# Kernel tuning notes

Hardware: AMD Instinct MI355X
Metric: run time of the kernel (lower is better)

The kernel has to match this reference:

```python
import jax, jax.numpy as jnp
import numpy as np

DEPTH = 4
HIDDEN = 256
ATOM_FDIM = 143
BOND_FDIM = 14
N_ATOMS = 65536
N_BONDS = 131072
MAX_NB = 6
ATOMS_PER_MOL = 32


def setup_inputs() -> dict:
    key = jax.random.key(0)
    ks = jax.random.split(key, 12)
    s = 0.05  # weight init scale
    return {
        'fatoms': jax.random.uniform(ks[0], (N_ATOMS, ATOM_FDIM), dtype=jnp.float32),
        'fbonds': jax.random.uniform(ks[1], (N_BONDS, ATOM_FDIM + BOND_FDIM), dtype=jnp.float32),
        'agraph': jax.random.randint(ks[2], (N_ATOMS, MAX_NB), 0, N_BONDS, dtype=jnp.int32),
        'bgraph': jax.random.randint(ks[3], (N_BONDS, MAX_NB), 0, N_BONDS, dtype=jnp.int32),
        'atoms_per_mol': ATOMS_PER_MOL,
        'W_i': jax.random.normal(ks[4], (ATOM_FDIM + BOND_FDIM, HIDDEN), dtype=jnp.float32) * s,
        'W_h': jax.random.normal(ks[5], (HIDDEN, HIDDEN), dtype=jnp.float32) * s,
        'W_o_w': jax.random.normal(ks[6], (ATOM_FDIM + HIDDEN, HIDDEN), dtype=jnp.float32) * s,
        'W_o_b': jax.random.normal(ks[7], (HIDDEN,), dtype=jnp.float32) * s,
        'W_a': jax.random.normal(ks[8], (HIDDEN, HIDDEN), dtype=jnp.float32) * s,
        'W_b_w': jax.random.normal(ks[9], (HIDDEN, HIDDEN), dtype=jnp.float32) * s,
        'W_b_b': jax.random.normal(ks[10], (HIDDEN,), dtype=jnp.float32) * s,
        'W_ma1': jax.random.normal(ks[11], (HIDDEN, 1), dtype=jnp.float32) * s,
    }


def reference(fatoms, fbonds, agraph, bgraph, atoms_per_mol,
              W_i, W_h, W_o_w, W_o_b, W_a, W_b_w, W_b_b, W_ma1):
    act = jax.nn.relu  # activation == 'ReLU'; dropout == 0 (identity)

    binput = fbonds @ W_i                      # [E, H]
    message = act(binput)
    for _ in range(DEPTH - 1):
        nei = message[bgraph]                  # [E, max_nb, H] gather
        # message attention over incoming messages (softmax over neighbor axis)
        att = jax.nn.softmax(nei @ W_ma1, axis=1)  # [E, max_nb, 1]
        nei = (nei * att).sum(axis=1)          # [E, H]
        message = act(binput + nei @ W_h)

    nei_a = message[agraph].sum(axis=1)        # [N, H]
    ainput = jnp.concatenate([fatoms, nei_a], axis=1)
    atom_h = act(ainput @ W_o_w + W_o_b)       # [N, H]

    # per-molecule self-attention pooling; equal-size molecules -> batched
    A = atoms_per_mol
    B = atom_h.shape[0] // A
    h = atom_h.reshape(B, A, HIDDEN)           # [B, A, H]
    scores = jnp.einsum('bad,bcd->bac', h @ W_a, h)   # [B, A, A]
    att_w = jax.nn.softmax(scores, axis=-1)
    att_h = act(jnp.einsum('bac,bcd->bad', att_w, h) @ W_b_w + W_b_b)
    mol_vecs = (h + att_h).sum(axis=1) / A     # [B, H]
    return mol_vecs
```

## Files before the change

kernel.cpp:

```cpp
#include <hip/hip_runtime.h>

typedef unsigned short u16;
typedef __attribute__((ext_vector_type(8))) short short8;
typedef __attribute__((ext_vector_type(4))) float floatx4;
typedef __attribute__((ext_vector_type(4), aligned(4))) float floatx4u;

__device__ __forceinline__ float bf2f(u16 u) {
    return __uint_as_float(((unsigned int)u) << 16);
}
__device__ __forceinline__ u16 f2bf(float f) {
    unsigned int i = __float_as_uint(f);
    unsigned int r = i + 0x7FFFu + ((i >> 16) & 1u);
    return (u16)(r >> 16);
}
__device__ __forceinline__ unsigned int relu2(unsigned int x) {
    unsigned int m = (((x >> 15) & 1u) * 0x0000FFFFu) | ((x >> 31) * 0xFFFF0000u);
    return x & ~m;
}

typedef __attribute__((address_space(3))) void lds_void;
typedef const __attribute__((address_space(1))) void g_void;
__device__ __forceinline__ void async_copy16(const void* g, void* l) {
    __builtin_amdgcn_global_load_lds((g_void*)g, (lds_void*)l, 16, 0, 0);
}

__device__ __forceinline__ void acc_bf8(float* a8, uint4 u, float wj) {
    a8[0] += wj * __uint_as_float(u.x << 16);
    a8[1] += wj * __uint_as_float(u.x & 0xffff0000u);
    a8[2] += wj * __uint_as_float(u.y << 16);
    a8[3] += wj * __uint_as_float(u.y & 0xffff0000u);
    a8[4] += wj * __uint_as_float(u.z << 16);
    a8[5] += wj * __uint_as_float(u.z & 0xffff0000u);
    a8[6] += wj * __uint_as_float(u.w << 16);
    a8[7] += wj * __uint_as_float(u.w & 0xffff0000u);
}

#define MFMA16(a, b, c) __builtin_amdgcn_mfma_f32_16x16x32_bf16(a, b, c, 0, 0, 0)

#define E_BONDS 131072
#define N_ATOMS_C 65536
#define KPAD_I 160
#define KPAD_O 416
#define N_MOLS 2048

__global__ __launch_bounds__(256) void prep_wt(const float* __restrict__ W, u16* __restrict__ Wt, int K, int Kpad) {
    int idx = blockIdx.x * 256 + threadIdx.x;
    int n = idx / Kpad;
    int k = idx - n * Kpad;
    float v = (k < K) ? W[(size_t)k * 256 + n] : 0.f;
    Wt[idx] = f2bf(v);
}

__global__ __launch_bounds__(256) void prep_wo(const float* __restrict__ W, u16* __restrict__ Wt) {
    int idx = blockIdx.x * 256 + threadIdx.x;
    int n = idx / KPAD_O;
    int k = idx - n * KPAD_O;
    float v = 0.f;
    if (k < 256)      v = W[(size_t)(143 + k) * 256 + n];
    else if (k < 399) v = W[(size_t)(k - 256) * 256 + n];
    Wt[idx] = f2bf(v);
}

template <int EPI, bool RELUA, bool F32A>
__global__ __launch_bounds__(512, 3) void gemm256(
    const u16* __restrict__ A, const u16* __restrict__ Bt,
    u16* __restrict__ out,
    const float* __restrict__ bias, const float* __restrict__ wma,
    float* __restrict__ tout, int K, const float* __restrict__ Af32)
{
    __shared__ char ldsbuf[33792];
    u16* Al = (u16*)ldsbuf;
    u16* Bl = (u16*)(ldsbuf + 8192);

    const int tid = threadIdx.x;
    const int w = tid >> 6, lane = tid & 63;
    const int quad = lane >> 4, mr = lane & 15;
    const int m0 = blockIdx.x * 128;

    floatx4 acc[16] = {};

    const u16* Ag = F32A ? nullptr : (A + (size_t)(m0 + (tid & 127)) * K + ((tid >> 7) << 3));
    const float* Af = F32A ? (Af32 + (size_t)(m0 + (tid >> 2)) * 157) : nullptr;

    for (int k0 = 0; k0 < K; k0 += 32) {
        if (F32A) {
            const int kb = tid & 3;
            const int cb = k0 + kb * 8;
            short8 xv;
            if (cb + 8 <= 157) {
                floatx4u v0 = *(const floatx4u*)(Af + cb);
                floatx4u v1 = *(const floatx4u*)(Af + cb + 4);
                xv[0] = (short)f2bf(v0.x); xv[1] = (short)f2bf(v0.y);
                xv[2] = (short)f2bf(v0.z); xv[3] = (short)f2bf(v0.w);
                xv[4] = (short)f2bf(v1.x); xv[5] = (short)f2bf(v1.y);
                xv[6] = (short)f2bf(v1.z); xv[7] = (short)f2bf(v1.w);
            } else {
#pragma unroll
                for (int e = 0; e < 8; ++e) {
                    int c = cb + e;
                    float v = (c < 157) ? Af[c] : 0.f;
                    xv[e] = (short)f2bf(v);
                }
            }
            *(short8*)(Al + ((kb << 7) + (tid >> 2)) * 8) = xv;
        } else if (RELUA) {
            uint4 x = *(const uint4*)(Ag + k0);
            x.x = relu2(x.x); x.y = relu2(x.y); x.z = relu2(x.z); x.w = relu2(x.w);
            *(uint4*)(Al + tid * 8) = x;
        } else {
            async_copy16(Ag + k0, Al + tid * 8);
        }
#pragma unroll
        for (int i = 0; i < 2; ++i) {
            int c = tid + i * 512;
            async_copy16(Bt + (size_t)(c & 255) * K + k0 + ((c >> 8) << 3), Bl + c * 8);
        }
        __syncthreads();

        short8 af = *(const short8*)(Al + quad * 1024 + (w * 16 + mr) * 8);
#pragma unroll
        for (int j = 0; j < 16; ++j) {
            short8 bf = *(const short8*)(Bl + quad * 2048 + (j * 16 + mr) * 8);
            acc[j] = MFMA16(af, bf, acc[j]);
        }
        __syncthreads();
    }

    u16* slice = (u16*)ldsbuf + w * 2112;
    const int lhalf = lane >> 5;
    const int lcol = (lane & 31) * 8;
    float wmal8[8];
    if (EPI == 1) {
#pragma unroll
        for (int e = 0; e < 8; ++e) wmal8[e] = wma[lcol + e];
    }
    float bl16[16];
    if (EPI == 3) {
#pragma unroll
        for (int j = 0; j < 16; ++j) bl16[j] = bias[j * 16 + mr];
    }

#pragma unroll
    for (int p = 0; p < 2; ++p) {
        if ((quad >> 1) == p) {
            int lr = (quad & 1) * 4;
#pragma unroll
            for (int j = 0; j < 16; ++j)
#pragma unroll
                for (int r = 0; r < 4; ++r) {
                    float v = acc[j][r];
                    if (EPI == 3) { v += bl16[j]; v = v > 0.f ? v : 0.f; }
                    slice[(lr + r) * 264 + j * 16 + mr] = f2bf(v);
                }
        }
        __syncthreads();
#pragma unroll
        for (int round = 0; round < 4; ++round) {
            int rowl = round * 2 + lhalf;
            int row = m0 + w * 16 + p * 8 + rowl;
            size_t off = (size_t)row * 256 + lcol;
            short8 pv = *(const short8*)(slice + rowl * 264 + lcol);
            if (EPI == 0 || EPI == 3) {
                *(short8*)(out + off) = pv;
            } else {
                *(short8*)(out + off) = pv;
                float pdot = 0.f;
#pragma unroll
                for (int e = 0; e < 8; ++e) {
                    u16 u = (u16)pv[e];
                    u = (u & 0x8000u) ? (u16)0 : u;
                    pdot += bf2f(u) * wmal8[e];
                }
                pdot += __shfl_xor(pdot, 1); pdot += __shfl_xor(pdot, 2);
                pdot += __shfl_xor(pdot, 4); pdot += __shfl_xor(pdot, 8);
                pdot += __shfl_xor(pdot, 16);
                if ((lane & 31) == 0) tout[row] = pdot;
            }
        }
        __syncthreads();
    }
}

template <int MODE>
__global__ __launch_bounds__(512, 6) void fused_gg(
    const u16* src, const u16* __restrict__ Bt, const int* __restrict__ graph,
    const float* __restrict__ t_in, const u16* __restrict__ binput,
    const float* __restrict__ fatoms, const float* __restrict__ bias,
    const float* __restrict__ wma, u16* __restrict__ outp, float* __restrict__ t_out)
{
    constexpr int MT = (MODE == 2) ? 32 : 64;
    constexpr int KK = (MODE == 2) ? 416 : 256;
    constexpr int KP = KK + 8;
    constexpr int MF = MT / 16;
    constexpr int LDSB = (MODE == 2) ? (32 * 424 * 2) : (32 * 268 * 4);

    __shared__ __align__(16) char ldsbuf[LDSB];
    u16* As = (u16*)ldsbuf;

    const int tid = threadIdx.x;
    const int w = tid >> 6, lane = tid & 63;
    const int quad = lane >> 4, mr = lane & 15;
    const int hw = tid >> 5, l32 = tid & 31;
    const int m0 = blockIdx.x * MT;

    for (int it = 0; it < MT / 16; ++it) {
        const int r = it * 16 + hw;
        const int e = m0 + r;
        const int* bg = graph + (size_t)e * 6;
        int2 b01 = *(const int2*)bg;
        int2 b23 = *(const int2*)(bg + 2);
        int2 b45 = *(const int2*)(bg + 4);
        int b[6] = {b01.x, b01.y, b23.x, b23.y, b45.x, b45.y};

        float wg[6];
        if (MODE != 2) {
            float s[6];
#pragma unroll
            for (int j = 0; j < 6; ++j) s[j] = t_in[b[j]];
            float mx = fmaxf(fmaxf(fmaxf(s[0], s[1]), fmaxf(s[2], s[3])), fmaxf(s[4], s[5]));
            float den = 0.f;
#pragma unroll
            for (int j = 0; j < 6; ++j) { wg[j] = __expf(s[j] - mx); den += wg[j]; }
            float inv = 1.f / den;
#pragma unroll
            for (int j = 0; j < 6; ++j) wg[j] *= inv;
        }

        float a8[8] = {};
#pragma unroll
        for (int j = 0; j < 6; ++j) {
            uint4 u = *(const uint4*)(src + (size_t)b[j] * 256 + l32 * 8);
            if (MODE == 1) { u.x = relu2(u.x); u.y = relu2(u.y); u.z = relu2(u.z); u.w = relu2(u.w); }
            acc_bf8(a8, u, (MODE == 2) ? 1.f : wg[j]);
        }
        short8 mv;
#pragma unroll
        for (int k = 0; k < 8; ++k) mv[k] = (short)f2bf(a8[k]);
        *(short8*)(As + r * KP + l32 * 8) = mv;

        if (MODE == 2) {
            const float* frow = fatoms + (size_t)e * 143;
#pragma unroll
            for (int i = 0; i < 5; ++i) {
                int c = l32 + i * 32;
                As[r * KP + 256 + c] = (c < 143) ? f2bf(frow[c]) : (u16)0;
            }
        }
    }
    __syncthreads();

    floatx4 acc[MF][2] = {};
    const u16* bp0 = Bt + (size_t)(w * 32 + mr) * KK + quad * 8;
    const u16* bp1 = bp0 + (size_t)16 * KK;
#pragma unroll 2
    for (int ks = 0; ks < KK / 32; ++ks) {
        const int k0 = ks * 32;
        short8 bf0 = *(const short8*)(bp0 + k0);
        short8 bf1 = *(const short8*)(bp1 + k0);
#pragma unroll
        for (int mf = 0; mf < MF; ++mf) {
            short8 af = *(const short8*)(As + (mf * 16 + mr) * KP + k0 + quad * 8);
            acc[mf][0] = MFMA16(af, bf0, acc[mf][0]);
            acc[mf][1] = MFMA16(af, bf1, acc[mf][1]);
        }
    }
    __syncthreads();

    if (MODE != 2) {
        float* Pf = (float*)ldsbuf;
        const int rrow = tid >> 4;
        const int rcol = (tid & 15) * 16;
        float wv[16];
#pragma unroll
        for (int e2 = 0; e2 < 16; ++e2) wv[e2] = wma[rcol + e2];

#pragma unroll
        for (int p = 0; p < 2; ++p) {
#pragma unroll
            for (int mi = 0; mi < 2; ++mi) {
#pragma unroll
                for (int jj = 0; jj < 2; ++jj)
#pragma unroll
                    for (int r = 0; r < 4; ++r)
                        Pf[(mi * 16 + quad * 4 + r) * 268 + (w * 2 + jj) * 16 + mr] = acc[p * 2 + mi][jj][r];
            }
            __syncthreads();
            const int grow = m0 + p * 32 + rrow;
            const u16* brow = binput + (size_t)grow * 256 + rcol;
            uint4 bu0 = *(const uint4*)brow;
            uint4 bu1 = *(const uint4*)(brow + 8);
            float bv[16] = {
                __uint_as_float(bu0.x << 16), __uint_as_float(bu0.x & 0xffff0000u),
                __uint_as_float(bu0.y << 16), __uint_as_float(bu0.y & 0xffff0000u),
                __uint_as_float(bu0.z << 16), __uint_as_float(bu0.z & 0xffff0000u),
                __uint_as_float(bu0.w << 16), __uint_as_float(bu0.w & 0xffff0000u),
                __uint_as_float(bu1.x << 16), __uint_as_float(bu1.x & 0xffff0000u),
                __uint_as_float(bu1.y << 16), __uint_as_float(bu1.y & 0xffff0000u),
                __uint_as_float(bu1.z << 16), __uint_as_float(bu1.z & 0xffff0000u),
                __uint_as_float(bu1.w << 16), __uint_as_float(bu1.w & 0xffff0000u)};
            const float* prow = Pf + rrow * 268 + rcol;
            float pdot = 0.f;
            short8 o0, o1;
#pragma unroll
            for (int e2 = 0; e2 < 16; ++e2) {
                float v = prow[e2] + bv[e2];
                v = v > 0.f ? v : 0.f;
                u16 q = f2bf(v);
                if (e2 < 8) o0[e2] = (short)q; else o1[e2 - 8] = (short)q;
                pdot += bf2f(q) * wv[e2];
            }
            size_t off = (size_t)grow * 256 + rcol;
            *(short8*)(outp + off) = o0;
            *(short8*)(outp + off + 8) = o1;
            pdot += __shfl_xor(pdot, 1); pdot += __shfl_xor(pdot, 2);
            pdot += __shfl_xor(pdot, 4); pdot += __shfl_xor(pdot, 8);
            if ((lane & 15) == 0) t_out[grow] = pdot;
            __syncthreads();
        }
    } else {
        u16* Pu = (u16*)ldsbuf;
        float bl0 = bias[(w * 2 + 0) * 16 + mr];
        float bl1 = bias[(w * 2 + 1) * 16 + mr];
#pragma unroll
        for (int mf = 0; mf < MF; ++mf)
#pragma unroll
            for (int r = 0; r < 4; ++r) {
                float v0 = acc[mf][0][r] + bl0; v0 = v0 > 0.f ? v0 : 0.f;
                float v1 = acc[mf][1][r] + bl1; v1 = v1 > 0.f ? v1 : 0.f;
                Pu[(mf * 16 + quad * 4 + r) * 264 + (w * 2 + 0) * 16 + mr] = f2bf(v0);
                Pu[(mf * 16 + quad * 4 + r) * 264 + (w * 2 + 1) * 16 + mr] = f2bf(v1);
            }
        __syncthreads();
        const int rrow = tid >> 4;
        const int rcol = (tid & 15) * 16;
        size_t off = (size_t)(m0 + rrow) * 256 + rcol;
        short8 v0 = *(const short8*)(Pu + rrow * 264 + rcol);
        short8 v1 = *(const short8*)(Pu + rrow * 264 + rcol + 8);
        *(short8*)(outp + off) = v0;
        *(short8*)(outp + off + 8) = v1;
    }
}

#define HSTR 260
__global__ __launch_bounds__(256) void mol_attn(const u16* __restrict__ atomh, const u16* __restrict__ hWg,
                                                u16* __restrict__ z) {
    __shared__ float hs[32 * HSTR];
    __shared__ float P[32 * 33];
    const int t = threadIdx.x;
    const int b = blockIdx.x;
    const u16* hbase = atomh + (size_t)b * 32 * 256;
    for (int e0 = t * 4; e0 < 8192; e0 += 1024) {
        int row = e0 >> 8, col = e0 & 255;
        ushort4 u = *(const ushort4*)(hbase + e0);
        floatx4 v; v.x = bf2f(u.x); v.y = bf2f(u.y); v.z = bf2f(u.z); v.w = bf2f(u.w);
        *(floatx4*)&hs[row * HSTR + col] = v;
    }
    __syncthreads();

    {
        int c = t & 31, a0 = t >> 5;
        const u16* hWb = hWg + (size_t)b * 32 * 256;
        for (int r = 0; r < 4; ++r) {
            int a = a0 + r * 8;
            const u16* hwrow = hWb + a * 256;
            float s = 0.f;
            for (int d = 0; d < 256; d += 4) {
                ushort4 u = *(const ushort4*)(hwrow + d);
                const float* hp = &hs[c * HSTR + d];
                s += bf2f(u.x) * hp[0] + bf2f(u.y) * hp[1] + bf2f(u.z) * hp[2] + bf2f(u.w) * hp[3];
            }
            P[a * 33 + c] = s;
        }
    }
    __syncthreads();
    if (t < 32) {
        float* prow = &P[t * 33];
        float mx = prow[0];
        for (int i = 1; i < 32; ++i) mx = fmaxf(mx, prow[i]);
        float den = 0.f;
        for (int i = 0; i < 32; ++i) { float ev = __expf(prow[i] - mx); prow[i] = ev; den += ev; }
        float inv = 1.f / den;
        for (int i = 0; i < 32; ++i) prow[i] *= inv;
    }
    __syncthreads();

    {
        int a = t >> 3, q = t & 7;
        floatx4 acc8[8];
#pragma unroll
        for (int i = 0; i < 8; ++i) acc8[i] = (floatx4){0.f, 0.f, 0.f, 0.f};
        const float* prow = &P[a * 33];
        for (int cc = 0; cc < 32; ++cc) {
            float p = prow[cc];
            const float* hrow = &hs[cc * HSTR + q * 4];
#pragma unroll
            for (int i = 0; i < 8; ++i) {
                floatx4 hv = *(const floatx4*)(hrow + i * 32);
                acc8[i] += p * hv;
            }
        }
        u16* zrow = z + ((size_t)b * 32 + a) * 256 + q * 4;
#pragma unroll
        for (int i = 0; i < 8; ++i) {
            ushort4 o;
            o.x = f2bf(acc8[i].x); o.y = f2bf(acc8[i].y); o.z = f2bf(acc8[i].z); o.w = f2bf(acc8[i].w);
            *(ushort4*)(zrow + i * 32) = o;
        }
    }
}

__global__ __launch_bounds__(256) void final_reduce(const u16* __restrict__ atomh, const u16* __restrict__ atth,
                                                    float* __restrict__ out) {
    int idx = blockIdx.x * 256 + threadIdx.x;
    int b = idx >> 8, d = idx & 255;
    const u16* ph = atomh + ((size_t)b * 32) * 256 + d;
    const u16* pa = atth + ((size_t)b * 32) * 256 + d;
    float s = 0.f;
#pragma unroll 4
    for (int a = 0; a < 32; ++a) s += bf2f(ph[a * 256]) + bf2f(pa[a * 256]);
    out[idx] = s * 0.03125f;
}

#define O_FBP      ((size_t)0)
#define O_BINPUT   ((size_t)41943040)
#define O_MSGA     ((size_t)109051904)
#define O_MSGB     ((size_t)176160768)
#define O_W        ((size_t)243269632)
#define O_WTI      (O_W)
#define O_WTH      (O_W + 81920)
#define O_WTO      (O_W + 212992)
#define O_WTA      (O_W + 425984)
#define O_WTB      (O_W + 557056)
#define WS_NEED    ((size_t)243957760)

extern "C" void kernel_launch(void* const* d_in, const int* in_sizes, int n_in,
                              void* d_out, int out_size, void* d_ws, size_t ws_size,
                              hipStream_t stream) {
    const float* fatoms = (const float*)d_in[0];
    const float* fbonds = (const float*)d_in[1];
    const int*   agraph = (const int*)d_in[2];
    const int*   bgraph = (const int*)d_in[3];
    const float* W_i    = (const float*)d_in[5];
    const float* W_h    = (const float*)d_in[6];
    const float* W_o_w  = (const float*)d_in[7];
    const float* W_o_b  = (const float*)d_in[8];
    const float* W_a    = (const float*)d_in[9];
    const float* W_b_w  = (const float*)d_in[10];
    const float* W_b_b  = (const float*)d_in[11];
    const float* W_ma1  = (const float*)d_in[12];
    float* out = (float*)d_out;

    if (ws_size < WS_NEED) return;

    char* ws = (char*)d_ws;
    u16* binput  = (u16*)(ws + O_BINPUT);
    u16* msgA    = (u16*)(ws + O_MSGA);
    u16* msgB    = (u16*)(ws + O_MSGB);
    u16* wti     = (u16*)(ws + O_WTI);
    u16* wth     = (u16*)(ws + O_WTH);
    u16* wto     = (u16*)(ws + O_WTO);
    u16* wta     = (u16*)(ws + O_WTA);
    u16* wtb     = (u16*)(ws + O_WTB);
    u16* atomh   = (u16*)(ws + O_FBP);
    u16* hW      = (u16*)(ws + O_BINPUT);
    u16* zbuf    = (u16*)(ws + O_BINPUT + 33554432);
    u16* atth    = (u16*)(ws + O_MSGA);
    float* tA = (float*)d_out;
    float* tB = tA + E_BONDS;

    prep_wt<<<160, 256, 0, stream>>>(W_i, wti, 157, KPAD_I);
    prep_wt<<<256, 256, 0, stream>>>(W_h, wth, 256, 256);
    prep_wo<<<416, 256, 0, stream>>>(W_o_w, wto);
    prep_wt<<<256, 256, 0, stream>>>(W_a, wta, 256, 256);
    prep_wt<<<256, 256, 0, stream>>>(W_b_w, wtb, 256, 256);

    gemm256<1, false, true><<<1024, 512, 0, stream>>>(nullptr, wti, binput, nullptr, W_ma1, tA, KPAD_I, fbonds);

    fused_gg<1><<<E_BONDS / 64, 512, 0, stream>>>(binput, wth, bgraph, tA, binput, nullptr, nullptr, W_ma1, msgA, tB);
    fused_gg<0><<<E_BONDS / 64, 512, 0, stream>>>(msgA,   wth, bgraph, tB, binput, nullptr, nullptr, W_ma1, msgB, tA);
    fused_gg<0><<<E_BONDS / 64, 512, 0, stream>>>(msgB,   wth, bgraph, tA, binput, nullptr, nullptr, W_ma1, msgA, tB);

    fused_gg<2><<<N_ATOMS_C / 32, 512, 0, stream>>>(msgA, wto, agraph, nullptr, nullptr, fatoms, W_o_b, nullptr, atomh, nullptr);

    gemm256<0, false, false><<<512, 512, 0, stream>>>(atomh, wta, hW, nullptr, nullptr, nullptr, 256, nullptr);
    mol_attn<<<N_MOLS, 256, 0, stream>>>(atomh, hW, zbuf);
    gemm256<3, false, false><<<512, 512, 0, stream>>>(zbuf, wtb, atth, W_b_b, nullptr, nullptr, 256, nullptr);

    final_reduce<<<N_MOLS, 256, 0, stream>>>(atomh, atth, out);
}
```

Measured before the change: 660.5 us.

## Fuse W_a projection into atom kernel and W_b GEMM plus pooling into mol_attn

The atom-output kernel now also multiplies its freshly computed atom_h tile (kept in LDS) by W_a and writes hW, which removes a separate GEMM launch and a reload of atom_h. The molecule attention kernel now keeps z in LDS, runs the W_b projection with MFMA, applies bias and ReLU, and reduces both h and att_h per molecule straight into the output. This drops two GEMM launches, the final reduce kernel, and the global round trips for z and att_h. In exchange the atom kernel does extra MFMA work per block with its B fragments read directly from global memory, and mol_attn2 uses more LDS, which may lower occupancy.

```diff
diff --git a/kernel.cpp b/kernel.cpp
--- a/kernel.cpp
+++ b/kernel.cpp
@@ -186,7 +186,8 @@
     const u16* src, const u16* __restrict__ Bt, const int* __restrict__ graph,
     const float* __restrict__ t_in, const u16* __restrict__ binput,
     const float* __restrict__ fatoms, const float* __restrict__ bias,
-    const float* __restrict__ wma, u16* __restrict__ outp, float* __restrict__ t_out)
+    const float* __restrict__ wma, u16* __restrict__ outp, float* __restrict__ t_out,
+    const u16* __restrict__ Bt2, u16* __restrict__ out2)
 {
     constexpr int MT = (MODE == 2) ? 32 : 64;
     constexpr int KK = (MODE == 2) ? 416 : 256;
@@ -331,23 +332,60 @@
                 Pu[(mf * 16 + quad * 4 + r) * 264 + (w * 2 + 1) * 16 + mr] = f2bf(v1);
             }
         __syncthreads();
-        const int rrow = tid >> 4;
-        const int rcol = (tid & 15) * 16;
-        size_t off = (size_t)(m0 + rrow) * 256 + rcol;
-        short8 v0 = *(const short8*)(Pu + rrow * 264 + rcol);
-        short8 v1 = *(const short8*)(Pu + rrow * 264 + rcol + 8);
-        *(short8*)(outp + off) = v0;
-        *(short8*)(outp + off + 8) = v1;
+        {
+            const int rrow = tid >> 4;
+            const int rcol = (tid & 15) * 16;
+            size_t off = (size_t)(m0 + rrow) * 256 + rcol;
+            *(short8*)(outp + off)     = *(const short8*)(Pu + rrow * 264 + rcol);
+            *(short8*)(outp + off + 8) = *(const short8*)(Pu + rrow * 264 + rcol + 8);
+        }
+
+        floatx4 acc2[2][2] = {};
+        const u16* cp0 = Bt2 + (size_t)(w * 32 + mr) * 256 + quad * 8;
+        const u16* cp1 = cp0 + (size_t)16 * 256;
+#pragma unroll 2
+        for (int ks = 0; ks < 8; ++ks) {
+            const int k0 = ks * 32;
+            short8 bf0 = *(const short8*)(cp0 + k0);
+            short8 bf1 = *(const short8*)(cp1 + k0);
+#pragma unroll
+            for (int mf = 0; mf < 2; ++mf) {
+                short8 af = *(const short8*)(Pu + (mf * 16 + mr) * 264 + k0 + quad * 8);
+                acc2[mf][0] = MFMA16(af, bf0, acc2[mf][0]);
+                acc2[mf][1] = MFMA16(af, bf1, acc2[mf][1]);
+            }
+        }
+        __syncthreads();
+#pragma unroll
+        for (int mf = 0; mf < 2; ++mf)
+#pragma unroll
+            for (int jj = 0; jj < 2; ++jj)
+#pragma unroll
+                for (int r = 0; r < 4; ++r)
+                    Pu[(mf * 16 + quad * 4 + r) * 264 + (w * 2 + jj) * 16 + mr] = f2bf(acc2[mf][jj][r]);
+        __syncthreads();
+        {
+            const int rrow = tid >> 4;
+            const int rcol = (tid & 15) * 16;
+            size_t off = (size_t)(m0 + rrow) * 256 + rcol;
+            *(short8*)(out2 + off)     = *(const short8*)(Pu + rrow * 264 + rcol);
+            *(short8*)(out2 + off + 8) = *(const short8*)(Pu + rrow * 264 + rcol + 8);
+        }
     }
 }
 
 #define HSTR 260
-__global__ __launch_bounds__(256) void mol_attn(const u16* __restrict__ atomh, const u16* __restrict__ hWg,
-                                                u16* __restrict__ z) {
+__global__ __launch_bounds__(256) void mol_attn2(const u16* __restrict__ atomh, const u16* __restrict__ hWg,
+                                                 const u16* __restrict__ wtb, const float* __restrict__ bb,
+                                                 float* __restrict__ out) {
     __shared__ float hs[32 * HSTR];
     __shared__ float P[32 * 33];
+    __shared__ u16 zl[32 * 264];
+    __shared__ float hsum[256];
+    __shared__ float attsum[256];
     const int t = threadIdx.x;
     const int b = blockIdx.x;
+    const int lane = t & 63, quad = lane >> 4, mr = lane & 15, w = t >> 6;
     const u16* hbase = atomh + (size_t)b * 32 * 256;
     for (int e0 = t * 4; e0 < 8192; e0 += 1024) {
         int row = e0 >> 8, col = e0 & 255;
@@ -399,26 +437,62 @@
                 acc8[i] += p * hv;
             }
         }
-        u16* zrow = z + ((size_t)b * 32 + a) * 256 + q * 4;
+        u16* zrow = zl + a * 264 + q * 4;
 #pragma unroll
         for (int i = 0; i < 8; ++i) {
             ushort4 o;
             o.x = f2bf(acc8[i].x); o.y = f2bf(acc8[i].y); o.z = f2bf(acc8[i].z); o.w = f2bf(acc8[i].w);
             *(ushort4*)(zrow + i * 32) = o;
         }
-    }
-}
-
-__global__ __launch_bounds__(256) void final_reduce(const u16* __restrict__ atomh, const u16* __restrict__ atth,
-                                                    float* __restrict__ out) {
-    int idx = blockIdx.x * 256 + threadIdx.x;
-    int b = idx >> 8, d = idx & 255;
-    const u16* ph = atomh + ((size_t)b * 32) * 256 + d;
-    const u16* pa = atth + ((size_t)b * 32) * 256 + d;
-    float s = 0.f;
-#pragma unroll 4
-    for (int a = 0; a < 32; ++a) s += bf2f(ph[a * 256]) + bf2f(pa[a * 256]);
-    out[idx] = s * 0.03125f;
+        float s = 0.f;
+        for (int aa = 0; aa < 32; ++aa) s += hs[aa * HSTR + t];
+        hsum[t] = s;
+    }
+    __syncthreads();
+
+    {
+        floatx4 acc2[2][4] = {};
+        const u16* bp[4];
+        float blw[4];
+#pragma unroll
+        for (int jj = 0; jj < 4; ++jj) {
+            int col = w * 64 + jj * 16 + mr;
+            bp[jj] = wtb + (size_t)col * 256 + quad * 8;
+            blw[jj] = bb[col];
+        }
+#pragma unroll 2
+        for (int ks = 0; ks < 8; ++ks) {
+            const int k0 = ks * 32;
+            short8 bf0 = *(const short8*)(bp[0] + k0);
+            short8 bf1 = *(const short8*)(bp[1] + k0);
+            short8 bf2v = *(const short8*)(bp[2] + k0);
+            short8 bf3 = *(const short8*)(bp[3] + k0);
+#pragma unroll
+            for (int mf = 0; mf < 2; ++mf) {
+                short8 af = *(const short8*)(zl + (mf * 16 + mr) * 264 + k0 + quad * 8);
+                acc2[mf][0] = MFMA16(af, bf0, acc2[mf][0]);
+                acc2[mf][1] = MFMA16(af, bf1, acc2[mf][1]);
+                acc2[mf][2] = MFMA16(af, bf2v, acc2[mf][2]);
+                acc2[mf][3] = MFMA16(af, bf3, acc2[mf][3]);
+            }
+        }
+#pragma unroll
+        for (int jj = 0; jj < 4; ++jj) {
+            float s = 0.f;
+#pragma unroll
+            for (int mf = 0; mf < 2; ++mf)
+#pragma unroll
+                for (int r = 0; r < 4; ++r) {
+                    float v = acc2[mf][jj][r] + blw[jj];
+                    s += (v > 0.f ? v : 0.f);
+                }
+            s += __shfl_xor(s, 16);
+            s += __shfl_xor(s, 32);
+            if (quad == 0) attsum[w * 64 + jj * 16 + mr] = s;
+        }
+    }
+    __syncthreads();
+    out[(size_t)b * 256 + t] = (hsum[t] + attsum[t]) * 0.03125f;
 }
 
 #define O_FBP      ((size_t)0)
@@ -463,8 +537,6 @@
     u16* wtb     = (u16*)(ws + O_WTB);
     u16* atomh   = (u16*)(ws + O_FBP);
     u16* hW      = (u16*)(ws + O_BINPUT);
-    u16* zbuf    = (u16*)(ws + O_BINPUT + 33554432);
-    u16* atth    = (u16*)(ws + O_MSGA);
     float* tA = (float*)d_out;
     float* tB = tA + E_BONDS;
 
@@ -476,15 +548,11 @@
 
     gemm256<1, false, true><<<1024, 512, 0, stream>>>(nullptr, wti, binput, nullptr, W_ma1, tA, KPAD_I, fbonds);
 
-    fused_gg<1><<<E_BONDS / 64, 512, 0, stream>>>(binput, wth, bgraph, tA, binput, nullptr, nullptr, W_ma1, msgA, tB);
-    fused_gg<0><<<E_BONDS / 64, 512, 0, stream>>>(msgA,   wth, bgraph, tB, binput, nullptr, nullptr, W_ma1, msgB, tA);
-    fused_gg<0><<<E_BONDS / 64, 512, 0, stream>>>(msgB,   wth, bgraph, tA, binput, nullptr, nullptr, W_ma1, msgA, tB);
-
-    fused_gg<2><<<N_ATOMS_C / 32, 512, 0, stream>>>(msgA, wto, agraph, nullptr, nullptr, fatoms, W_o_b, nullptr, atomh, nullptr);
-
-    gemm256<0, false, false><<<512, 512, 0, stream>>>(atomh, wta, hW, nullptr, nullptr, nullptr, 256, nullptr);
-    mol_attn<<<N_MOLS, 256, 0, stream>>>(atomh, hW, zbuf);
-    gemm256<3, false, false><<<512, 512, 0, stream>>>(zbuf, wtb, atth, W_b_b, nullptr, nullptr, 256, nullptr);
-
-    final_reduce<<<N_MOLS, 256, 0, stream>>>(atomh, atth, out);
-}
+    fused_gg<1><<<E_BONDS / 64, 512, 0, stream>>>(binput, wth, bgraph, tA, binput, nullptr, nullptr, W_ma1, msgA, tB, nullptr, nullptr);
+    fused_gg<0><<<E_BONDS / 64, 512, 0, stream>>>(msgA,   wth, bgraph, tB, binput, nullptr, nullptr, W_ma1, msgB, tA, nullptr, nullptr);
+    fused_gg<0><<<E_BONDS / 64, 512, 0, stream>>>(msgB,   wth, bgraph, tA, binput, nullptr, nullptr, W_ma1, msgA, tB, nullptr, nullptr);
+
+    fused_gg<2><<<N_ATOMS_C / 32, 512, 0, stream>>>(msgA, wto, agraph, nullptr, nullptr, fatoms, W_o_b, nullptr, atomh, nullptr, wta, hW);
+
+    mol_attn2<<<N_MOLS, 256, 0, stream>>>(atomh, hW, wtb, W_b_b, out);
+}
```

After: 678.2 us. +2.7%, slower.
